# Kernel optimization log

Measured on AMD Instinct MI355X. Metric: run time of the kernel, lower is better.

The kernel has to match this reference:

```python
import jax, jax.numpy as jnp
import numpy as np

N_HEADS = 16


def setup_inputs() -> dict:
    key = jax.random.key(0)
    k1, k2, k3, k4 = jax.random.split(key, 4)
    B, T, C = 2, 2048, 1024
    x = jax.random.normal(k1, (B, T, C), dtype=jnp.float32)
    scale = 1.0 / np.sqrt(C)
    Wq = jax.random.normal(k2, (C, C), dtype=jnp.float32) * scale
    Wk = jax.random.normal(k3, (C, C), dtype=jnp.float32) * scale
    Wv = jax.random.normal(k4, (C, C), dtype=jnp.float32) * scale
    return {"x": x, "Wq": Wq, "Wk": Wk, "Wv": Wv}


def reference(x, Wq, Wk, Wv):
    B, T, C = x.shape
    H = N_HEADS
    Dh = C // H
    # Faithful to original: direct view of (B,T,C) -> (B,H,T,Dh) (no transpose)
    q = (x @ Wq.T).reshape(B, H, T, Dh)
    k = (x @ Wk.T).reshape(B, H, T, Dh)
    v = (x @ Wv.T).reshape(B, H, T, Dh)
    scores = jnp.einsum('bhqd,bhkd->bhqk', q, k) * (1.0 / (Dh ** 0.5))
    mask = jnp.tril(jnp.ones((T, T), dtype=bool))  # causal mask
    scores = jnp.where(mask, scores, -jnp.inf)
    att = jax.nn.softmax(scores, axis=-1)
    out = jnp.einsum('bhqk,bhkd->bhqd', att, v)
    return out.reshape(B, T, C)
```

## Files before the change

### kernel.cpp

```cpp
#include <hip/hip_runtime.h>
#include <hip/hip_bf16.h>
#include <stdint.h>

#define AS1 __attribute__((address_space(1)))
#define AS3 __attribute__((address_space(3)))

typedef __bf16 bf16x8 __attribute__((ext_vector_type(8)));
typedef float  f32x4  __attribute__((ext_vector_type(4)));
typedef unsigned short ushort8v __attribute__((ext_vector_type(8)));
typedef unsigned short ushort4v __attribute__((ext_vector_type(4)));
typedef short short8v __attribute__((ext_vector_type(8)));
typedef short short4v __attribute__((ext_vector_type(4)));

__device__ __forceinline__ unsigned short f2bf(float f) {
    unsigned int u = __float_as_uint(f);
    u += 0x7fffu + ((u >> 16) & 1u);
    return (unsigned short)(u >> 16);
}
__device__ __forceinline__ unsigned int pk2bf(float a, float b) {
    __hip_bfloat162 h = __float22bfloat162_rn(make_float2(a, b));
    unsigned int u;
    __builtin_memcpy(&u, &h, 4);
    return u;
}
__device__ __forceinline__ void g2lds16(const void* gp, void* lp) {
    __builtin_amdgcn_global_load_lds((AS1 void*)gp, (AS3 void*)lp, 16, 0, 0);
}
#define E2(x) __builtin_amdgcn_exp2f(x)

__global__ __launch_bounds__(256) void cast_all(const float* __restrict__ x,
                                                const float* __restrict__ w0,
                                                const float* __restrict__ w1,
                                                const float* __restrict__ w2,
                                                unsigned short* __restrict__ xb,
                                                unsigned short* __restrict__ wc) {
    int id = blockIdx.x;
    const float* s;
    unsigned short* d;
    int base;
    if (id < 4096) { s = x; d = xb; base = id; }
    else {
        int z = (id - 4096) >> 10;
        s = (z == 0) ? w0 : (z == 1) ? w1 : w2;
        d = wc + (size_t)z * 1048576;
        base = (id - 4096) & 1023;
    }
    int i = (base * 256 + threadIdx.x) * 4;
    float4 v = *(const float4*)(s + i);
    ushort4v o = { f2bf(v.x), f2bf(v.y), f2bf(v.z), f2bf(v.w) };
    *(ushort4v*)(d + i) = o;
}

#define VMW(n) asm volatile("s_waitcnt vmcnt(" #n ")" ::: "memory")
#define NOW
#define PHCORE(STG, MFMAS, ENDW) do {                                          \
    STG;                                                                       \
    __builtin_amdgcn_s_barrier();                                              \
    asm volatile("s_waitcnt lgkmcnt(0)" ::: "memory");                         \
    __builtin_amdgcn_sched_barrier(0);                                         \
    __builtin_amdgcn_s_setprio(1);                                             \
    MFMAS;                                                                     \
    __builtin_amdgcn_s_setprio(0);                                             \
    __builtin_amdgcn_sched_barrier(0);                                         \
    ENDW;                                                                      \
    __builtin_amdgcn_s_barrier();                                              \
} while (0)

#define PHA(S, CUR, STG, ENDW) do {                                            \
    const int kx_ = ((S) * 32 + quad * 8) ^ ((cl & 7) * 8);                    \
    bf16x8 af_[4];                                                             \
    _Pragma("unroll")                                                          \
    for (int m_ = 0; m_ < 4; ++m_)                                             \
        af_[m_] = *(const bf16x8*)&SA[CUR][(rowA0 + m_ * 16) * 64 + kx_];      \
    _Pragma("unroll")                                                          \
    for (int n_ = 0; n_ < 4; ++n_)                                             \
        bqr[n_] = *(const bf16x8*)&SB[CUR][(rowB0 + n_ * 16) * 64 + kx_];      \
    PHCORE(STG,                                                                \
        _Pragma("unroll")                                                      \
        for (int m_ = 0; m_ < 4; ++m_)                                         \
            _Pragma("unroll")                                                  \
            for (int n_ = 0; n_ < 4; ++n_)                                     \
                acc[m_][n_] = __builtin_amdgcn_mfma_f32_16x16x32_bf16(         \
                    af_[m_], bqr[n_], acc[m_][n_], 0, 0, 0);                   \
        , ENDW);                                                               \
} while (0)

#define PHB(S, CUR, STG, ENDW) do {                                            \
    const int kx_ = ((S) * 32 + quad * 8) ^ ((cl & 7) * 8);                    \
    bf16x8 af_[4];                                                             \
    _Pragma("unroll")                                                          \
    for (int m_ = 0; m_ < 4; ++m_)                                             \
        af_[m_] = *(const bf16x8*)&SA[CUR][(rowA0 + 64 + m_ * 16) * 64 + kx_]; \
    PHCORE(STG,                                                                \
        _Pragma("unroll")                                                      \
        for (int m_ = 0; m_ < 4; ++m_)                                         \
            _Pragma("unroll")                                                  \
            for (int n_ = 0; n_ < 4; ++n_)                                     \
                acc[4 + m_][n_] = __builtin_amdgcn_mfma_f32_16x16x32_bf16(     \
                    af_[m_], bqr[n_], acc[4 + m_][n_], 0, 0, 0);               \
        , ENDW);                                                               \
} while (0)

__global__ __launch_bounds__(512, 2) void gemm_qkv(const unsigned short* __restrict__ X,
                                                   const unsigned short* __restrict__ W,
                                                   unsigned short* __restrict__ QKV) {
    const int K = 1024, N = 1024;
    const int b = blockIdx.x;
    const int z = b >> 6;
    const int r = b & 63;
    const int m0 = (r >> 2) * 256;
    const int n0 = (r & 3) * 256;

    const unsigned short* A = X;
    const unsigned short* Bp = W + (size_t)z * (1024 * 1024);
    unsigned short* C = QKV + (size_t)z * (4096 * 1024);
    const float qs = (z == 0) ? 0.18033688011112042f : 1.0f;

    __shared__ unsigned short SA[2][16384];
    __shared__ unsigned short SB[2][16384];

    const int t = threadIdx.x;
    const int w = t >> 6;
    const int l = t & 63;
    const int cl = l & 15;
    const int quad = l >> 4;
    const int rowA0 = (w >> 2) * 128 + cl;
    const int rowB0 = (w & 3) * 64 + cl;

    const int srow8 = t >> 3;
    const int klog = (((t & 7) ^ ((t >> 3) & 7)) * 8);
    const unsigned short* Abase = A + (size_t)(m0 + srow8) * K + klog;
    const unsigned short* Bbase = Bp + (size_t)(n0 + srow8) * K + klog;
    unsigned short* const sa0 = &SA[0][w * 512];
    unsigned short* const sa1 = &SA[1][w * 512];
    unsigned short* const sb0 = &SB[0][w * 512];
    unsigned short* const sb1 = &SB[1][w * 512];

    f32x4 acc[8][4] = {};
    bf16x8 bqr[4];

#define STGA(nb, q, k0) g2lds16(Abase + (size_t)(q) * 65536 + (k0), ((nb) ? sa1 : sa0) + (q) * 4096)
#define STGB(nb, q, k0) g2lds16(Bbase + (size_t)(q) * 65536 + (k0), ((nb) ? sb1 : sb0) + (q) * 4096)

    STGB(0, 0, 0); STGB(0, 1, 0); STGB(0, 2, 0); STGB(0, 3, 0);
    STGA(0, 0, 0); STGA(0, 2, 0); STGA(0, 1, 0); STGA(0, 3, 0);
    VMW(2);
    __builtin_amdgcn_s_barrier();

    for (int tt = 0; tt < 15; ++tt) {
        const int cur = tt & 1, nxt = cur ^ 1;
        const int k1 = (tt + 1) * 64;
        PHA(0, cur, { STGB(nxt, 0, k1); STGB(nxt, 1, k1); }, VMW(2));
        PHB(0, cur, { STGB(nxt, 2, k1); STGB(nxt, 3, k1); }, NOW);
        PHA(1, cur, { STGA(nxt, 0, k1); STGA(nxt, 2, k1); }, NOW);
        PHB(1, cur, { STGA(nxt, 1, k1); STGA(nxt, 3, k1); }, VMW(2));
    }
    PHA(0, 1, {}, VMW(0));
    PHB(0, 1, {}, NOW);
    PHA(1, 1, {}, NOW);
    PHB(1, 1, {}, NOW);

#undef STGA
#undef STGB

    #pragma unroll
    for (int mf = 0; mf < 8; ++mf) {
        #pragma unroll
        for (int rr = 0; rr < 4; ++rr) {
            size_t row = (size_t)(m0 + (w >> 2) * 128 + mf * 16 + quad * 4 + rr);
            #pragma unroll
            for (int nf = 0; nf < 4; ++nf)
                C[row * N + (n0 + (w & 3) * 64 + nf * 16 + cl)] = f2bf(acc[mf][nf][rr] * qs);
        }
    }
}

__global__ __launch_bounds__(256) void vtrans(const unsigned short* __restrict__ Vn,
                                              unsigned short* __restrict__ V3) {
    const int bh = blockIdx.y;
    const int T0 = blockIdx.x * 128;
    __shared__ unsigned short L[128 * 72];
    const int t = threadIdx.x;

    const unsigned short* src = Vn + (size_t)bh * 131072 + (size_t)T0 * 64;
    #pragma unroll
    for (int p = 0; p < 4; ++p) {
        int r = p * 32 + (t >> 3), c = (t & 7) * 8;
        *(ushort8v*)(L + r * 72 + c) = *(const ushort8v*)(src + (size_t)r * 64 + c);
    }
    __syncthreads();
    unsigned short* dst = V3 + (size_t)bh * 131072 + (size_t)(T0 >> 4) * 1024;
    #pragma unroll
    for (int p = 0; p < 2; ++p) {
        int item = p * 256 + t;
        int kb = item >> 6, cl = (item >> 2) & 15, qk = item & 3;
        ushort8v a, b;
        #pragma unroll
        for (int u = 0; u < 8; ++u) {
            int dt = u >> 2, j = u & 3;
            a[u] = L[(kb * 16 + qk * 4 + j) * 72 + dt * 16 + cl];
            b[u] = L[(kb * 16 + qk * 4 + j) * 72 + (dt + 2) * 16 + cl];
        }
        unsigned short* dp = dst + kb * 1024 + cl * 64 + qk * 16;
        *(ushort8v*)(dp) = a;
        *(ushort8v*)(dp + 8) = b;
    }
}

__global__ __launch_bounds__(256, 4) void attn(const unsigned short* __restrict__ QK,
                                               const unsigned short* __restrict__ V3,
                                               float* __restrict__ Out) {
    const int id = blockIdx.x;
    const int bh = id & 31;
    const int bb = 31 - (id >> 5);
    const int t = threadIdx.x;
    const int w = t >> 6;
    const int l = t & 63;
    const int cl = l & 15;
    const int quad = l >> 4;
    const int c7 = cl & 7;

    const size_t bhoff = (size_t)bh * 131072;
    const unsigned short* Qb = QK + bhoff;
    const unsigned short* Kb = QK + (size_t)4194304 + bhoff;
    const unsigned short* Vb = V3 + bhoff;
    float* Ob = Out + bhoff;

    __shared__ unsigned short KVs[2][8192];

    const int g2 = t + 256;
    const int kO1 = (t >> 3) * 64 + (((t & 7) ^ ((t >> 3) & 7)) * 8);
    const int kO2 = (g2 >> 3) * 64 + (((g2 & 7) ^ ((g2 >> 3) & 7)) * 8);
    const int wg1 = t & 63;
    const int wg2 = g2 & 63;
    const int vO1 = (t >> 6) * 512 + ((wg1 ^ ((wg1 >> 3) & 7)) * 8);
    const int vO2 = (g2 >> 6) * 512 + ((wg2 ^ ((wg2 >> 3) & 7)) * 8);
    const int lB1 = w * 512;
    const int lB2 = 2048 + w * 512;

    const int oK0 = cl * 64 + (((quad)     ^ c7) * 8);
    const int oK1 = cl * 64 + (((quad + 4) ^ c7) * 8);
    const int oV0 = cl * 64 + (((quad * 2)     ^ c7) * 8);
    const int oV1 = cl * 64 + (((quad * 2 + 1) ^ c7) * 8);

    const int mrel = w * 16 + cl;
    const int nch = bb + 1;
    const int m0w = bb * 64 + w * 16;

    bf16x8 qf0, qf1;
    {
        const unsigned short* qa = Qb + (size_t)(m0w + cl) * 64 + quad * 8;
        qf0 = *(const bf16x8*)(qa);
        qf1 = *(const bf16x8*)(qa + 32);
    }

    f32x4 o[4] = {};
    float lps = 0.f;

    {
        unsigned short* s = &KVs[0][0];
        g2lds16(Kb + kO1, s + lB1);
        g2lds16(Kb + kO2, s + lB2);
        g2lds16(Vb + vO1, s + 4096 + lB1);
        g2lds16(Vb + vO2, s + 4096 + lB2);
    }

    for (int c = 0; c < nch; ++c) {
        __syncthreads();
        if (c + 1 < nch) {
            unsigned short* s = &KVs[(c + 1) & 1][0];
            const size_t off = (size_t)(c + 1) * 4096;
            g2lds16(Kb + off + kO1, s + lB1);
            g2lds16(Kb + off + kO2, s + lB2);
            g2lds16(Vb + off + vO1, s + 4096 + lB1);
            g2lds16(Vb + off + vO2, s + 4096 + lB2);
        }
        const unsigned short* Kl = &KVs[c & 1][0];
        const unsigned short* Vl = Kl + 4096;
        const bool masked = (c == bb);

        bf16x8 kf0[4], kf1[4];
        #pragma unroll
        for (int kt = 0; kt < 4; ++kt) {
            kf0[kt] = *(const bf16x8*)(Kl + kt * 1024 + oK0);
            kf1[kt] = *(const bf16x8*)(Kl + kt * 1024 + oK1);
        }
        f32x4 st[4] = {};
        __builtin_amdgcn_s_setprio(1);
        #pragma unroll
        for (int kt = 0; kt < 4; ++kt) {
            st[kt] = __builtin_amdgcn_mfma_f32_16x16x32_bf16(kf0[kt], qf0, st[kt], 0, 0, 0);
            st[kt] = __builtin_amdgcn_mfma_f32_16x16x32_bf16(kf1[kt], qf1, st[kt], 0, 0, 0);
        }
        __builtin_amdgcn_s_setprio(0);

        short4v pb[4];
        #pragma unroll
        for (int kt = 0; kt < 4; ++kt) {
            float p0, p1, p2, p3;
            if (masked) {
                const int lk = kt * 16 + quad * 4;
                p0 = (lk     <= mrel) ? E2(st[kt][0]) : 0.f;
                p1 = (lk + 1 <= mrel) ? E2(st[kt][1]) : 0.f;
                p2 = (lk + 2 <= mrel) ? E2(st[kt][2]) : 0.f;
                p3 = (lk + 3 <= mrel) ? E2(st[kt][3]) : 0.f;
            } else {
                p0 = E2(st[kt][0]);
                p1 = E2(st[kt][1]);
                p2 = E2(st[kt][2]);
                p3 = E2(st[kt][3]);
            }
            lps += (p0 + p1) + (p2 + p3);
            uint2 u = { pk2bf(p0, p1), pk2bf(p2, p3) };
            short4v pv;
            __builtin_memcpy(&pv, &u, 8);
            pb[kt] = pv;
        }

        __builtin_amdgcn_s_setprio(1);
        #pragma unroll
        for (int kt = 0; kt < 4; ++kt) {
            short8v v0 = *(const short8v*)(Vl + kt * 1024 + oV0);
            short8v v1 = *(const short8v*)(Vl + kt * 1024 + oV1);
            short4v a0 = __builtin_shufflevector(v0, v0, 0, 1, 2, 3);
            short4v a1 = __builtin_shufflevector(v0, v0, 4, 5, 6, 7);
            short4v a2 = __builtin_shufflevector(v1, v1, 0, 1, 2, 3);
            short4v a3 = __builtin_shufflevector(v1, v1, 4, 5, 6, 7);
            o[0] = __builtin_amdgcn_mfma_f32_16x16x16bf16_1k(a0, pb[kt], o[0], 0, 0, 0);
            o[1] = __builtin_amdgcn_mfma_f32_16x16x16bf16_1k(a1, pb[kt], o[1], 0, 0, 0);
            o[2] = __builtin_amdgcn_mfma_f32_16x16x16bf16_1k(a2, pb[kt], o[2], 0, 0, 0);
            o[3] = __builtin_amdgcn_mfma_f32_16x16x16bf16_1k(a3, pb[kt], o[3], 0, 0, 0);
        }
        __builtin_amdgcn_s_setprio(0);
    }

    lps += __shfl_xor(lps, 16);
    lps += __shfl_xor(lps, 32);
    const float inv = 1.0f / lps;
    #pragma unroll
    for (int dt = 0; dt < 4; ++dt) {
        f32x4 r = o[dt];
        r[0] *= inv; r[1] *= inv; r[2] *= inv; r[3] *= inv;
        *(f32x4*)(Ob + (size_t)(m0w + cl) * 64 + dt * 16 + quad * 4) = r;
    }
}

extern "C" void kernel_launch(void* const* d_in, const int* in_sizes, int n_in,
                              void* d_out, int out_size, void* d_ws, size_t ws_size,
                              hipStream_t stream) {
    const float* x  = (const float*)d_in[0];
    const float* Wq = (const float*)d_in[1];
    const float* Wk = (const float*)d_in[2];
    const float* Wv = (const float*)d_in[3];
    float* out = (float*)d_out;

    unsigned short* xb  = (unsigned short*)d_ws;
    unsigned short* wc  = xb + (size_t)4096 * 1024;
    unsigned short* qkv = wc + (size_t)3 * 1024 * 1024;
    unsigned short* vt  = qkv + (size_t)3 * 4096 * 1024;

    hipLaunchKernelGGL(cast_all, dim3(7168), dim3(256), 0, stream, x, Wq, Wk, Wv, xb, wc);
    hipLaunchKernelGGL(gemm_qkv, dim3(192), dim3(512), 0, stream, xb, wc, qkv);
    hipLaunchKernelGGL(vtrans, dim3(16, 32), dim3(256), 0, stream, qkv + (size_t)2 * 4096 * 1024, vt);
    hipLaunchKernelGGL(attn, dim3(1024), dim3(256), 0, stream, qkv, vt, out);
}
```

Measured before the change: 145.8 us.

## Use two waves per attention block, each covering 32 query rows

Shrinks the attention block from four waves to two, with each wave now handling two 16-row query tiles. Each K/V fragment read from shared memory is reused for twice as many MFMAs, which cuts LDS read traffic per unit of compute. Each thread now issues four async global-to-LDS loads per K and V chunk instead of two. The cost is more registers per wave (double the accumulators and scores), fewer waves to hide latency, and a changed launch bound that may lower occupancy.

```diff
diff --git a/kernel.cpp b/kernel.cpp
--- a/kernel.cpp
+++ b/kernel.cpp
@@ -207,7 +207,7 @@
     }
 }
 
-__global__ __launch_bounds__(256, 4) void attn(const unsigned short* __restrict__ QK,
+__global__ __launch_bounds__(128, 2) void attn(const unsigned short* __restrict__ QK,
                                                const unsigned short* __restrict__ V3,
                                                float* __restrict__ Out) {
     const int id = blockIdx.x;
@@ -228,41 +228,38 @@
 
     __shared__ unsigned short KVs[2][8192];
 
-    const int g2 = t + 256;
-    const int kO1 = (t >> 3) * 64 + (((t & 7) ^ ((t >> 3) & 7)) * 8);
-    const int kO2 = (g2 >> 3) * 64 + (((g2 & 7) ^ ((g2 >> 3) & 7)) * 8);
-    const int wg1 = t & 63;
-    const int wg2 = g2 & 63;
-    const int vO1 = (t >> 6) * 512 + ((wg1 ^ ((wg1 >> 3) & 7)) * 8);
-    const int vO2 = (g2 >> 6) * 512 + ((wg2 ^ ((wg2 >> 3) & 7)) * 8);
-    const int lB1 = w * 512;
-    const int lB2 = 2048 + w * 512;
+    const int kOb = (t >> 3) * 64 + (((t & 7) ^ ((t >> 3) & 7)) * 8);
+    const int vOb = (t >> 6) * 512 + (((t & 63) ^ ((t >> 3) & 7)) * 8);
+    const int lB = w * 512;
 
     const int oK0 = cl * 64 + (((quad)     ^ c7) * 8);
     const int oK1 = cl * 64 + (((quad + 4) ^ c7) * 8);
     const int oV0 = cl * 64 + (((quad * 2)     ^ c7) * 8);
     const int oV1 = cl * 64 + (((quad * 2 + 1) ^ c7) * 8);
 
-    const int mrel = w * 16 + cl;
     const int nch = bb + 1;
-    const int m0w = bb * 64 + w * 16;
-
-    bf16x8 qf0, qf1;
-    {
-        const unsigned short* qa = Qb + (size_t)(m0w + cl) * 64 + quad * 8;
-        qf0 = *(const bf16x8*)(qa);
-        qf1 = *(const bf16x8*)(qa + 32);
-    }
-
-    f32x4 o[4] = {};
-    float lps = 0.f;
+    const int m0w = bb * 64 + w * 32;
+    const int mrel0 = w * 32 + cl;
+    const int mrel1 = w * 32 + 16 + cl;
+
+    bf16x8 qf[2][2];
+    #pragma unroll
+    for (int qb = 0; qb < 2; ++qb) {
+        const unsigned short* qa = Qb + (size_t)(m0w + qb * 16 + cl) * 64 + quad * 8;
+        qf[qb][0] = *(const bf16x8*)(qa);
+        qf[qb][1] = *(const bf16x8*)(qa + 32);
+    }
+
+    f32x4 o0[4] = {}, o1[4] = {};
+    float lps0 = 0.f, lps1 = 0.f;
 
     {
         unsigned short* s = &KVs[0][0];
-        g2lds16(Kb + kO1, s + lB1);
-        g2lds16(Kb + kO2, s + lB2);
-        g2lds16(Vb + vO1, s + 4096 + lB1);
-        g2lds16(Vb + vO2, s + 4096 + lB2);
+        #pragma unroll
+        for (int i = 0; i < 4; ++i) {
+            g2lds16(Kb + i * 1024 + kOb, s + lB + i * 1024);
+            g2lds16(Vb + i * 1024 + vOb, s + 4096 + lB + i * 1024);
+        }
     }
 
     for (int c = 0; c < nch; ++c) {
@@ -270,10 +267,11 @@
         if (c + 1 < nch) {
             unsigned short* s = &KVs[(c + 1) & 1][0];
             const size_t off = (size_t)(c + 1) * 4096;
-            g2lds16(Kb + off + kO1, s + lB1);
-            g2lds16(Kb + off + kO2, s + lB2);
-            g2lds16(Vb + off + vO1, s + 4096 + lB1);
-            g2lds16(Vb + off + vO2, s + 4096 + lB2);
+            #pragma unroll
+            for (int i = 0; i < 4; ++i) {
+                g2lds16(Kb + off + i * 1024 + kOb, s + lB + i * 1024);
+                g2lds16(Vb + off + i * 1024 + vOb, s + 4096 + lB + i * 1024);
+            }
         }
         const unsigned short* Kl = &KVs[c & 1][0];
         const unsigned short* Vl = Kl + 4096;
@@ -285,36 +283,48 @@
             kf0[kt] = *(const bf16x8*)(Kl + kt * 1024 + oK0);
             kf1[kt] = *(const bf16x8*)(Kl + kt * 1024 + oK1);
         }
-        f32x4 st[4] = {};
+        f32x4 s0[4] = {}, s1[4] = {};
         __builtin_amdgcn_s_setprio(1);
         #pragma unroll
         for (int kt = 0; kt < 4; ++kt) {
-            st[kt] = __builtin_amdgcn_mfma_f32_16x16x32_bf16(kf0[kt], qf0, st[kt], 0, 0, 0);
-            st[kt] = __builtin_amdgcn_mfma_f32_16x16x32_bf16(kf1[kt], qf1, st[kt], 0, 0, 0);
+            s0[kt] = __builtin_amdgcn_mfma_f32_16x16x32_bf16(kf0[kt], qf[0][0], s0[kt], 0, 0, 0);
+            s0[kt] = __builtin_amdgcn_mfma_f32_16x16x32_bf16(kf1[kt], qf[0][1], s0[kt], 0, 0, 0);
+            s1[kt] = __builtin_amdgcn_mfma_f32_16x16x32_bf16(kf0[kt], qf[1][0], s1[kt], 0, 0, 0);
+            s1[kt] = __builtin_amdgcn_mfma_f32_16x16x32_bf16(kf1[kt], qf[1][1], s1[kt], 0, 0, 0);
         }
         __builtin_amdgcn_s_setprio(0);
 
-        short4v pb[4];
+        short4v pb0[4], pb1[4];
         #pragma unroll
         for (int kt = 0; kt < 4; ++kt) {
+            const int lk = kt * 16 + quad * 4;
             float p0, p1, p2, p3;
             if (masked) {
-                const int lk = kt * 16 + quad * 4;
-                p0 = (lk     <= mrel) ? E2(st[kt][0]) : 0.f;
-                p1 = (lk + 1 <= mrel) ? E2(st[kt][1]) : 0.f;
-                p2 = (lk + 2 <= mrel) ? E2(st[kt][2]) : 0.f;
-                p3 = (lk + 3 <= mrel) ? E2(st[kt][3]) : 0.f;
+                p0 = (lk     <= mrel0) ? E2(s0[kt][0]) : 0.f;
+                p1 = (lk + 1 <= mrel0) ? E2(s0[kt][1]) : 0.f;
+                p2 = (lk + 2 <= mrel0) ? E2(s0[kt][2]) : 0.f;
+                p3 = (lk + 3 <= mrel0) ? E2(s0[kt][3]) : 0.f;
             } else {
-                p0 = E2(st[kt][0]);
-                p1 = E2(st[kt][1]);
-                p2 = E2(st[kt][2]);
-                p3 = E2(st[kt][3]);
+                p0 = E2(s0[kt][0]); p1 = E2(s0[kt][1]);
+                p2 = E2(s0[kt][2]); p3 = E2(s0[kt][3]);
             }
-            lps += (p0 + p1) + (p2 + p3);
-            uint2 u = { pk2bf(p0, p1), pk2bf(p2, p3) };
-            short4v pv;
-            __builtin_memcpy(&pv, &u, 8);
-            pb[kt] = pv;
+            lps0 += (p0 + p1) + (p2 + p3);
+            uint2 u0 = { pk2bf(p0, p1), pk2bf(p2, p3) };
+            __builtin_memcpy(&pb0[kt], &u0, 8);
+
+            float r0, r1, r2, r3;
+            if (masked) {
+                r0 = (lk     <= mrel1) ? E2(s1[kt][0]) : 0.f;
+                r1 = (lk + 1 <= mrel1) ? E2(s1[kt][1]) : 0.f;
+                r2 = (lk + 2 <= mrel1) ? E2(s1[kt][2]) : 0.f;
+                r3 = (lk + 3 <= mrel1) ? E2(s1[kt][3]) : 0.f;
+            } else {
+                r0 = E2(s1[kt][0]); r1 = E2(s1[kt][1]);
+                r2 = E2(s1[kt][2]); r3 = E2(s1[kt][3]);
+            }
+            lps1 += (r0 + r1) + (r2 + r3);
+            uint2 u1 = { pk2bf(r0, r1), pk2bf(r2, r3) };
+            __builtin_memcpy(&pb1[kt], &u1, 8);
         }
 
         __builtin_amdgcn_s_setprio(1);
@@ -326,22 +336,32 @@
             short4v a1 = __builtin_shufflevector(v0, v0, 4, 5, 6, 7);
             short4v a2 = __builtin_shufflevector(v1, v1, 0, 1, 2, 3);
             short4v a3 = __builtin_shufflevector(v1, v1, 4, 5, 6, 7);
-            o[0] = __builtin_amdgcn_mfma_f32_16x16x16bf16_1k(a0, pb[kt], o[0], 0, 0, 0);
-            o[1] = __builtin_amdgcn_mfma_f32_16x16x16bf16_1k(a1, pb[kt], o[1], 0, 0, 0);
-            o[2] = __builtin_amdgcn_mfma_f32_16x16x16bf16_1k(a2, pb[kt], o[2], 0, 0, 0);
-            o[3] = __builtin_amdgcn_mfma_f32_16x16x16bf16_1k(a3, pb[kt], o[3], 0, 0, 0);
+            o0[0] = __builtin_amdgcn_mfma_f32_16x16x16bf16_1k(a0, pb0[kt], o0[0], 0, 0, 0);
+            o0[1] = __builtin_amdgcn_mfma_f32_16x16x16bf16_1k(a1, pb0[kt], o0[1], 0, 0, 0);
+            o0[2] = __builtin_amdgcn_mfma_f32_16x16x16bf16_1k(a2, pb0[kt], o0[2], 0, 0, 0);
+            o0[3] = __builtin_amdgcn_mfma_f32_16x16x16bf16_1k(a3, pb0[kt], o0[3], 0, 0, 0);
+            o1[0] = __builtin_amdgcn_mfma_f32_16x16x16bf16_1k(a0, pb1[kt], o1[0], 0, 0, 0);
+            o1[1] = __builtin_amdgcn_mfma_f32_16x16x16bf16_1k(a1, pb1[kt], o1[1], 0, 0, 0);
+            o1[2] = __builtin_amdgcn_mfma_f32_16x16x16bf16_1k(a2, pb1[kt], o1[2], 0, 0, 0);
+            o1[3] = __builtin_amdgcn_mfma_f32_16x16x16bf16_1k(a3, pb1[kt], o1[3], 0, 0, 0);
         }
         __builtin_amdgcn_s_setprio(0);
     }
 
-    lps += __shfl_xor(lps, 16);
-    lps += __shfl_xor(lps, 32);
-    const float inv = 1.0f / lps;
+    lps0 += __shfl_xor(lps0, 16);
+    lps0 += __shfl_xor(lps0, 32);
+    lps1 += __shfl_xor(lps1, 16);
+    lps1 += __shfl_xor(lps1, 32);
+    const float inv0 = 1.0f / lps0;
+    const float inv1 = 1.0f / lps1;
     #pragma unroll
     for (int dt = 0; dt < 4; ++dt) {
-        f32x4 r = o[dt];
-        r[0] *= inv; r[1] *= inv; r[2] *= inv; r[3] *= inv;
+        f32x4 r = o0[dt];
+        r[0] *= inv0; r[1] *= inv0; r[2] *= inv0; r[3] *= inv0;
         *(f32x4*)(Ob + (size_t)(m0w + cl) * 64 + dt * 16 + quad * 4) = r;
+        f32x4 q = o1[dt];
+        q[0] *= inv1; q[1] *= inv1; q[2] *= inv1; q[3] *= inv1;
+        *(f32x4*)(Ob + (size_t)(m0w + 16 + cl) * 64 + dt * 16 + quad * 4) = q;
     }
 }
 
@@ -362,5 +382,5 @@
     hipLaunchKernelGGL(cast_all, dim3(7168), dim3(256), 0, stream, x, Wq, Wk, Wv, xb, wc);
     hipLaunchKernelGGL(gemm_qkv, dim3(192), dim3(512), 0, stream, xb, wc, qkv);
     hipLaunchKernelGGL(vtrans, dim3(16, 32), dim3(256), 0, stream, qkv + (size_t)2 * 4096 * 1024, vt);
-    hipLaunchKernelGGL(attn, dim3(1024), dim3(256), 0, stream, qkv, vt, out);
-}
+    hipLaunchKernelGGL(attn, dim3(1024), dim3(128), 0, stream, qkv, vt, out);
+}
```

After: 156.0 us. +7.0%, slower.

## Retile QKV GEMM to 256x192 tiles over fused N=3072 for 256 blocks

Applied to the files above, without the earlier changes.

The QKV projection GEMM now treats the three weight matrices as one concatenated N=3072 output and uses 256x192 tiles instead of 256x256. This gives 256 workgroups instead of 192, which should fill the GPU's compute units more evenly and reduce wave-quantization tail. The cost is fewer MFMAs per LDS B load, a rebalanced staging schedule across phases, and a per-fragment Q/K/V selection in the epilogue.

```diff
diff --git a/kernel.cpp b/kernel.cpp
--- a/kernel.cpp
+++ b/kernel.cpp
@@ -73,13 +73,13 @@
     for (int m_ = 0; m_ < 4; ++m_)                                             \
         af_[m_] = *(const bf16x8*)&SA[CUR][(rowA0 + m_ * 16) * 64 + kx_];      \
     _Pragma("unroll")                                                          \
-    for (int n_ = 0; n_ < 4; ++n_)                                             \
+    for (int n_ = 0; n_ < 3; ++n_)                                             \
         bqr[n_] = *(const bf16x8*)&SB[CUR][(rowB0 + n_ * 16) * 64 + kx_];      \
     PHCORE(STG,                                                                \
         _Pragma("unroll")                                                      \
         for (int m_ = 0; m_ < 4; ++m_)                                         \
             _Pragma("unroll")                                                  \
-            for (int n_ = 0; n_ < 4; ++n_)                                     \
+            for (int n_ = 0; n_ < 3; ++n_)                                     \
                 acc[m_][n_] = __builtin_amdgcn_mfma_f32_16x16x32_bf16(         \
                     af_[m_], bqr[n_], acc[m_][n_], 0, 0, 0);                   \
         , ENDW);                                                               \
@@ -95,7 +95,7 @@
         _Pragma("unroll")                                                      \
         for (int m_ = 0; m_ < 4; ++m_)                                         \
             _Pragma("unroll")                                                  \
-            for (int n_ = 0; n_ < 4; ++n_)                                     \
+            for (int n_ = 0; n_ < 3; ++n_)                                     \
                 acc[4 + m_][n_] = __builtin_amdgcn_mfma_f32_16x16x32_bf16(     \
                     af_[m_], bqr[n_], acc[4 + m_][n_], 0, 0, 0);               \
         , ENDW);                                                               \
@@ -104,20 +104,15 @@
 __global__ __launch_bounds__(512, 2) void gemm_qkv(const unsigned short* __restrict__ X,
                                                    const unsigned short* __restrict__ W,
                                                    unsigned short* __restrict__ QKV) {
-    const int K = 1024, N = 1024;
+    const int K = 1024;
     const int b = blockIdx.x;
-    const int z = b >> 6;
-    const int r = b & 63;
-    const int m0 = (r >> 2) * 256;
-    const int n0 = (r & 3) * 256;
-
-    const unsigned short* A = X;
-    const unsigned short* Bp = W + (size_t)z * (1024 * 1024);
-    unsigned short* C = QKV + (size_t)z * (4096 * 1024);
-    const float qs = (z == 0) ? 0.18033688011112042f : 1.0f;
+    const int m0 = (b >> 4) * 256;
+    const int n0 = (b & 15) * 192;
+
+    const float qs0 = 0.18033688011112042f;
 
     __shared__ unsigned short SA[2][16384];
-    __shared__ unsigned short SB[2][16384];
+    __shared__ unsigned short SB[2][12288];
 
     const int t = threadIdx.x;
     const int w = t >> 6;
@@ -125,24 +120,24 @@
     const int cl = l & 15;
     const int quad = l >> 4;
     const int rowA0 = (w >> 2) * 128 + cl;
-    const int rowB0 = (w & 3) * 64 + cl;
+    const int rowB0 = (w & 3) * 48 + cl;
 
     const int srow8 = t >> 3;
     const int klog = (((t & 7) ^ ((t >> 3) & 7)) * 8);
-    const unsigned short* Abase = A + (size_t)(m0 + srow8) * K + klog;
-    const unsigned short* Bbase = Bp + (size_t)(n0 + srow8) * K + klog;
+    const unsigned short* Abase = X + (size_t)(m0 + srow8) * K + klog;
+    const unsigned short* Bbase = W + (size_t)(n0 + srow8) * K + klog;
     unsigned short* const sa0 = &SA[0][w * 512];
     unsigned short* const sa1 = &SA[1][w * 512];
     unsigned short* const sb0 = &SB[0][w * 512];
     unsigned short* const sb1 = &SB[1][w * 512];
 
-    f32x4 acc[8][4] = {};
-    bf16x8 bqr[4];
+    f32x4 acc[8][3] = {};
+    bf16x8 bqr[3];
 
 #define STGA(nb, q, k0) g2lds16(Abase + (size_t)(q) * 65536 + (k0), ((nb) ? sa1 : sa0) + (q) * 4096)
 #define STGB(nb, q, k0) g2lds16(Bbase + (size_t)(q) * 65536 + (k0), ((nb) ? sb1 : sb0) + (q) * 4096)
 
-    STGB(0, 0, 0); STGB(0, 1, 0); STGB(0, 2, 0); STGB(0, 3, 0);
+    STGB(0, 0, 0); STGB(0, 1, 0); STGB(0, 2, 0);
     STGA(0, 0, 0); STGA(0, 2, 0); STGA(0, 1, 0); STGA(0, 3, 0);
     VMW(2);
     __builtin_amdgcn_s_barrier();
@@ -151,9 +146,9 @@
         const int cur = tt & 1, nxt = cur ^ 1;
         const int k1 = (tt + 1) * 64;
         PHA(0, cur, { STGB(nxt, 0, k1); STGB(nxt, 1, k1); }, VMW(2));
-        PHB(0, cur, { STGB(nxt, 2, k1); STGB(nxt, 3, k1); }, NOW);
-        PHA(1, cur, { STGA(nxt, 0, k1); STGA(nxt, 2, k1); }, NOW);
-        PHB(1, cur, { STGA(nxt, 1, k1); STGA(nxt, 3, k1); }, VMW(2));
+        PHB(0, cur, { STGB(nxt, 2, k1); STGA(nxt, 0, k1); }, NOW);
+        PHA(1, cur, { STGA(nxt, 2, k1); STGA(nxt, 1, k1); }, NOW);
+        PHB(1, cur, { STGA(nxt, 3, k1); },                   VMW(2));
     }
     PHA(0, 1, {}, VMW(0));
     PHB(0, 1, {}, NOW);
@@ -169,8 +164,13 @@
         for (int rr = 0; rr < 4; ++rr) {
             size_t row = (size_t)(m0 + (w >> 2) * 128 + mf * 16 + quad * 4 + rr);
             #pragma unroll
-            for (int nf = 0; nf < 4; ++nf)
-                C[row * N + (n0 + (w & 3) * 64 + nf * 16 + cl)] = f2bf(acc[mf][nf][rr] * qs);
+            for (int nf = 0; nf < 3; ++nf) {
+                const int nbase = n0 + (w & 3) * 48 + nf * 16;
+                const int z = nbase >> 10;
+                const float qs = (z == 0) ? qs0 : 1.0f;
+                unsigned short* Cz = QKV + (size_t)z * 4194304;
+                Cz[row * 1024 + ((nbase & 1023) + cl)] = f2bf(acc[mf][nf][rr] * qs);
+            }
         }
     }
 }
@@ -360,7 +360,7 @@
     unsigned short* vt  = qkv + (size_t)3 * 4096 * 1024;
 
     hipLaunchKernelGGL(cast_all, dim3(7168), dim3(256), 0, stream, x, Wq, Wk, Wv, xb, wc);
-    hipLaunchKernelGGL(gemm_qkv, dim3(192), dim3(512), 0, stream, xb, wc, qkv);
+    hipLaunchKernelGGL(gemm_qkv, dim3(256), dim3(512), 0, stream, xb, wc, qkv);
     hipLaunchKernelGGL(vtrans, dim3(16, 32), dim3(256), 0, stream, qkv + (size_t)2 * 4096 * 1024, vt);
     hipLaunchKernelGGL(attn, dim3(1024), dim3(256), 0, stream, qkv, vt, out);
 }
```

Measured after the change: 143.0 us. Within noise of the previous version (-1.9%).
